# Kernel tuning notes

Hardware: AMD Instinct MI355X
Metric: run time of the kernel (lower is better)

The kernel has to match this reference:

```python
import jax, jax.numpy as jnp
import numpy as np

D_MODEL = 1024
NUM_HEADS = 16
D_K = D_MODEL // NUM_HEADS


def setup_inputs() -> dict:
    key = jax.random.key(0)
    ks = jax.random.split(key, 9)
    B, S = 2, 2048
    s_in = 1.0 / np.sqrt(D_MODEL)
    x = jax.random.normal(ks[0], (B, S, D_MODEL), dtype=jnp.float32)
    # Linear weights stored as (in_features, out_features): y = x @ W + b
    Wq = jax.random.uniform(ks[1], (D_MODEL, D_MODEL), jnp.float32, -s_in, s_in)
    bq = jax.random.uniform(ks[2], (D_MODEL,), jnp.float32, -s_in, s_in)
    Wk = jax.random.uniform(ks[3], (D_MODEL, D_K), jnp.float32, -s_in, s_in)
    bk = jax.random.uniform(ks[4], (D_K,), jnp.float32, -s_in, s_in)
    Wv = jax.random.uniform(ks[5], (D_MODEL, D_K), jnp.float32, -s_in, s_in)
    bv = jax.random.uniform(ks[6], (D_K,), jnp.float32, -s_in, s_in)
    Wo = jax.random.uniform(ks[7], (D_MODEL, D_MODEL), jnp.float32, -s_in, s_in)
    bo = jax.random.uniform(ks[8], (D_MODEL,), jnp.float32, -s_in, s_in)
    return {"x": x, "Wq": Wq, "bq": bq, "Wk": Wk, "bk": bk,
            "Wv": Wv, "bv": bv, "Wo": Wo, "bo": bo}


def reference(x, Wq, bq, Wk, bk, Wv, bv, Wo, bo):
    B, S, _ = x.shape
    H, Dk = NUM_HEADS, D_K
    # Projections
    Q = (x @ Wq + bq).reshape(B, S, H, Dk).transpose(0, 2, 1, 3)  # [B,H,S,Dk]
    K = x @ Wk + bk                                               # [B,S,Dk] single KV head
    V = x @ Wv + bv                                               # [B,S,Dk]
    # Scores: query heads broadcast against the single shared KV head
    scores = jnp.einsum('bhqd,bkd->bhqk', Q, K) / jnp.sqrt(jnp.float32(Dk))
    attn = jax.nn.softmax(scores, axis=-1)                        # [B,H,S,S]
    out = jnp.einsum('bhqk,bkd->bhqd', attn, V)                   # [B,H,S,Dk]
    out = out.transpose(0, 2, 1, 3).reshape(B, S, H * Dk)         # [B,S,d_model]
    return out @ Wo + bo
```

## Files before the change

### kernel.cpp

```cpp
#include <hip/hip_runtime.h>
#include <hip/hip_bf16.h>

typedef __attribute__((ext_vector_type(8))) short bf16x8;
typedef __attribute__((ext_vector_type(4))) float f32x4;
typedef __attribute__((ext_vector_type(16))) float f32x16;
typedef __attribute__((ext_vector_type(4))) unsigned short ushort4v;

#define QSCALE 0.1803368801111204f

__device__ __forceinline__ unsigned short f2bf(float f) {
  union { float f; unsigned int u; } x; x.f = f;
  unsigned int u = x.u;
  unsigned int r = (u + 0x7fffu + ((u >> 16) & 1u)) >> 16;
  return (unsigned short)r;
}

__device__ __forceinline__ void gll16(const unsigned short* g, unsigned short* l) {
  __builtin_amdgcn_global_load_lds(
      (const __attribute__((address_space(1))) unsigned int*)g,
      (__attribute__((address_space(3))) unsigned int*)l, 16, 0, 0);
}

__global__ __launch_bounds__(256) void prep_kernel(
    const float* __restrict__ x,
    const float* __restrict__ Wq, const float* __restrict__ Wk,
    const float* __restrict__ Wv, const float* __restrict__ Wo,
    unsigned short* __restrict__ xb,
    unsigned short* __restrict__ QKVt, unsigned short* __restrict__ Wot) {
  int z = blockIdx.z;
  if (z == 4) {
    size_t base = ((size_t)(blockIdx.y * 32 + blockIdx.x)) * 4096 + threadIdx.x * 16;
#pragma unroll
    for (int c = 0; c < 4; ++c) {
      float4 v = *(const float4*)(x + base + c * 4);
      ushort4v o = { f2bf(v.x), f2bf(v.y), f2bf(v.z), f2bf(v.w) };
      *(ushort4v*)(xb + base + c * 4) = o;
    }
    return;
  }
  __shared__ float t[32][33];
  const float* src;
  unsigned short* dst;
  int C, rowoff;
  if (z == 0)      { src = Wq; dst = QKVt; C = 1024; rowoff = 0; }
  else if (z == 1) { src = Wk; dst = QKVt; C = 64;   rowoff = 1024; }
  else if (z == 2) { src = Wv; dst = QKVt; C = 64;   rowoff = 1088; }
  else             { src = Wo; dst = Wot;  C = 1024; rowoff = 0; }
  int c0 = blockIdx.x * 32, r0 = blockIdx.y * 32;
  if (c0 >= C) return;
  int tx = threadIdx.x & 31, ty = threadIdx.x >> 5;
#pragma unroll
  for (int i = 0; i < 32; i += 8)
    t[ty + i][tx] = src[(size_t)(r0 + ty + i) * C + c0 + tx];
  __syncthreads();
#pragma unroll
  for (int i = 0; i < 32; i += 8)
    dst[(size_t)(rowoff + c0 + ty + i) * 1024 + r0 + tx] = f2bf(t[tx][ty + i]);
}

template <typename OutT, bool QKVMODE>
__global__ __launch_bounds__(256) void gemm_bf16_kernel(
    const unsigned short* __restrict__ A, const unsigned short* __restrict__ Bt,
    const float* __restrict__ b0, const float* __restrict__ b1,
    const float* __restrict__ b2, OutT* __restrict__ C,
    unsigned short* __restrict__ Vt, int M, int N, int K) {
  __shared__ __align__(16) unsigned short As[2][128 * 32];
  __shared__ __align__(16) unsigned short Bs[2][64 * 32];
  int tid = threadIdx.x;
  int wid = tid >> 6, lane = tid & 63;
  int l15 = lane & 15, quad = lane >> 4;
  int m0 = blockIdx.x * 128, n0 = blockIdx.y * 64;
  int mw = (wid >> 1) * 64, nw = (wid & 1) * 32;
  f32x4 acc[4][2];
#pragma unroll
  for (int i = 0; i < 4; i++)
#pragma unroll
    for (int j = 0; j < 2; j++)
#pragma unroll
      for (int e = 0; e < 4; ++e) acc[i][j][e] = 0.f;

  const unsigned short* Ag = A + (size_t)(m0 + (tid >> 2)) * K + (tid & 3) * 8;
  const unsigned short* Bg = Bt + (size_t)(n0 + (tid >> 2)) * K + (tid & 3) * 8;

  gll16(Ag, As[0] + tid * 8);
  gll16(Ag + (size_t)64 * K, As[0] + 2048 + tid * 8);
  gll16(Bg, Bs[0] + tid * 8);

  for (int k0 = 0; k0 < K; k0 += 32) {
    int cur = (k0 >> 5) & 1;
    if (k0 + 32 < K) {
      int nxt = cur ^ 1;
      gll16(Ag + k0 + 32, As[nxt] + tid * 8);
      gll16(Ag + (size_t)64 * K + k0 + 32, As[nxt] + 2048 + tid * 8);
      gll16(Bg + k0 + 32, Bs[nxt] + tid * 8);
      asm volatile("s_waitcnt vmcnt(3)" ::: "memory");
    } else {
      asm volatile("s_waitcnt vmcnt(0)" ::: "memory");
    }
    __builtin_amdgcn_s_barrier();
    __builtin_amdgcn_sched_barrier(0);
    const unsigned short* Asb = As[cur];
    const unsigned short* Bsb = Bs[cur];
    bf16x8 af[4], bfr[2];
#pragma unroll
    for (int t = 0; t < 4; ++t)
      af[t] = *(const bf16x8*)(Asb + (mw + t * 16 + l15) * 32 + quad * 8);
#pragma unroll
    for (int t = 0; t < 2; ++t)
      bfr[t] = *(const bf16x8*)(Bsb + (nw + t * 16 + l15) * 32 + quad * 8);
#pragma unroll
    for (int mt = 0; mt < 4; ++mt)
#pragma unroll
      for (int nt = 0; nt < 2; ++nt)
        acc[mt][nt] = __builtin_amdgcn_mfma_f32_16x16x32_bf16(
            af[mt], bfr[nt], acc[mt][nt], 0, 0, 0);
    asm volatile("s_waitcnt lgkmcnt(0)" ::: "memory");
    __builtin_amdgcn_sched_barrier(0);
    __builtin_amdgcn_s_barrier();
  }
#pragma unroll
  for (int mt = 0; mt < 4; ++mt)
#pragma unroll
    for (int nt = 0; nt < 2; ++nt) {
      int col = n0 + nw + nt * 16 + l15;
      float bias, cs;
      if constexpr (QKVMODE) {
        bias = (col < 1024) ? b0[col] : ((col < 1088) ? b1[col - 1024] : b2[col - 1088]);
        cs = (col < 1024) ? QSCALE : 1.0f;
      } else {
        bias = b0[col];
        cs = 1.0f;
      }
#pragma unroll
      for (int r = 0; r < 4; ++r) {
        int row = m0 + mw + mt * 16 + quad * 4 + r;
        float v = (acc[mt][nt][r] + bias) * cs;
        if constexpr (sizeof(OutT) == 2)
          C[(size_t)row * N + col] = f2bf(v);
        else
          C[(size_t)row * N + col] = v;
        if constexpr (QKVMODE) {
          if (col >= 1088)
            Vt[((size_t)(row >> 11) * 64 + (col - 1088)) * 2048 + (row & 2047)] =
                f2bf(v);
        }
      }
    }
}

__global__ __launch_bounds__(512, 4) void flash_attn_kernel(
    const unsigned short* __restrict__ QKV,
    const unsigned short* __restrict__ Vt,
    unsigned short* __restrict__ AO) {
  constexpr int S = 2048, LDQ = 1152;
  constexpr int PK = 72;
  __shared__ __align__(16) unsigned short smem[2][2][64 * PK];
  int tid = threadIdx.x;
  int wid = tid >> 6, lane = tid & 63;
  int l31 = lane & 31, half = lane >> 5;
  int p = wid & 3, ks = wid >> 2;
  int q0 = blockIdx.x * 128, h = blockIdx.y, b = blockIdx.z;

  const unsigned short* Qb =
      QKV + (size_t)(b * S + q0 + p * 32 + l31) * LDQ + h * 64 + half * 8;
  bf16x8 qf[4];
#pragma unroll
  for (int f = 0; f < 4; ++f) qf[f] = *(const bf16x8*)(Qb + f * 16);

  int u = tid & 255, sl = tid >> 8;
  int srow = u >> 2, sc = (u & 3) * 8;
  const unsigned short* Kgb = QKV + ((size_t)b * S) * LDQ + 1024;
  const unsigned short* Vgb = Vt + ((size_t)(b * 64 + srow)) * 2048;

  f32x16 oa0, oa1;
#pragma unroll
  for (int r = 0; r < 16; ++r) { oa0[r] = 0.f; oa1[r] = 0.f; }
  float rs = 0.f;

  int kb0 = sl * 1024;
  bf16x8 ka = *(const bf16x8*)(Kgb + (size_t)(kb0 + srow) * LDQ + sc);
  bf16x8 kc = *(const bf16x8*)(Kgb + (size_t)(kb0 + srow) * LDQ + sc + 32);
  bf16x8 va = *(const bf16x8*)(Vgb + kb0 + sc);
  bf16x8 vc = *(const bf16x8*)(Vgb + kb0 + sc + 32);

  unsigned short* Ksb = smem[ks][0];
  unsigned short* Vsb = smem[ks][1];

  for (int kt = 0; kt < 16; ++kt) {
    *(bf16x8*)(smem[sl][0] + srow * PK + sc) = ka;
    *(bf16x8*)(smem[sl][0] + srow * PK + sc + 32) = kc;
    *(bf16x8*)(smem[sl][1] + srow * PK + sc) = va;
    *(bf16x8*)(smem[sl][1] + srow * PK + sc + 32) = vc;
    __syncthreads();
    if (kt + 1 < 16) {
      int kbn = sl * 1024 + (kt + 1) * 64;
      ka = *(const bf16x8*)(Kgb + (size_t)(kbn + srow) * LDQ + sc);
      kc = *(const bf16x8*)(Kgb + (size_t)(kbn + srow) * LDQ + sc + 32);
      va = *(const bf16x8*)(Vgb + kbn + sc);
      vc = *(const bf16x8*)(Vgb + kbn + sc + 32);
    }

#pragma unroll
    for (int n2 = 0; n2 < 2; ++n2) {
      f32x16 sacc;
#pragma unroll
      for (int i = 0; i < 16; ++i) sacc[i] = 0.f;
#pragma unroll
      for (int s = 0; s < 4; ++s) {
        bf16x8 kf =
            *(const bf16x8*)(Ksb + (n2 * 32 + l31) * PK + s * 16 + half * 8);
        sacc = __builtin_amdgcn_mfma_f32_32x32x16_bf16(kf, qf[s], sacc, 0, 0, 0);
      }
#pragma unroll
      for (int t = 0; t < 2; ++t) {
        float pr[8];
#pragma unroll
        for (int j = 0; j < 8; ++j) {
          pr[j] = __builtin_amdgcn_exp2f(sacc[t * 8 + j]);
          rs += pr[j];
        }
        unsigned w0A, w1A, w0B, w1B;
        asm("v_cvt_pk_bf16_f32 %0, %1, %2" : "=v"(w0A) : "v"(pr[0]), "v"(pr[1]));
        asm("v_cvt_pk_bf16_f32 %0, %1, %2" : "=v"(w1A) : "v"(pr[2]), "v"(pr[3]));
        asm("v_cvt_pk_bf16_f32 %0, %1, %2" : "=v"(w0B) : "v"(pr[4]), "v"(pr[5]));
        asm("v_cvt_pk_bf16_f32 %0, %1, %2" : "=v"(w1B) : "v"(pr[6]), "v"(pr[7]));
        asm volatile("v_permlane32_swap_b32 %0, %1" : "+v"(w0A), "+v"(w0B));
        asm volatile("v_permlane32_swap_b32 %0, %1" : "+v"(w1A), "+v"(w1B));
        union { unsigned u[4]; bf16x8 v; } afu;
        afu.u[0] = w0A; afu.u[1] = w1A; afu.u[2] = w0B; afu.u[3] = w1B;
        int sg = n2 * 2 + t;
        bf16x8 vf0 = *(const bf16x8*)(Vsb + (l31) * PK + sg * 16 + half * 8);
        bf16x8 vf1 = *(const bf16x8*)(Vsb + (32 + l31) * PK + sg * 16 + half * 8);
        oa0 = __builtin_amdgcn_mfma_f32_32x32x16_bf16(afu.v, vf0, oa0, 0, 0, 0);
        oa1 = __builtin_amdgcn_mfma_f32_32x32x16_bf16(afu.v, vf1, oa1, 0, 0, 0);
      }
    }
    __syncthreads();
  }

  float rsf = rs + __shfl_xor(rs, 32, 64);

  float* Cb = (float*)smem;
  if (ks == 1) {
#pragma unroll
    for (int r = 0; r < 16; ++r) {
      int row = (r & 3) + 8 * (r >> 2) + 4 * half;
      Cb[(p * 32 + row) * 66 + l31] = oa0[r];
      Cb[(p * 32 + row) * 66 + 32 + l31] = oa1[r];
    }
    if (half == 0) Cb[(p * 32 + l31) * 66 + 64] = rsf;
  } else {
    if (half == 0) Cb[(p * 32 + l31) * 66 + 65] = rsf;
  }
  __syncthreads();
  if (ks == 0) {
    unsigned short* Ob = AO + (size_t)(b * S + q0 + p * 32) * 1024 + h * 64;
#pragma unroll
    for (int r = 0; r < 16; ++r) {
      int row = (r & 3) + 8 * (r >> 2) + 4 * half;
      float p0 = Cb[(p * 32 + row) * 66 + l31];
      float p1 = Cb[(p * 32 + row) * 66 + 32 + l31];
      float inv = 1.0f / (Cb[(p * 32 + row) * 66 + 64] + Cb[(p * 32 + row) * 66 + 65]);
      Ob[(size_t)row * 1024 + l31] = f2bf((oa0[r] + p0) * inv);
      Ob[(size_t)row * 1024 + 32 + l31] = f2bf((oa1[r] + p1) * inv);
    }
  }
}

extern "C" void kernel_launch(void* const* d_in, const int* in_sizes, int n_in,
                              void* d_out, int out_size, void* d_ws, size_t ws_size,
                              hipStream_t stream) {
  const float* x  = (const float*)d_in[0];
  const float* Wq = (const float*)d_in[1];
  const float* bq = (const float*)d_in[2];
  const float* Wk = (const float*)d_in[3];
  const float* bk = (const float*)d_in[4];
  const float* Wv = (const float*)d_in[5];
  const float* bv = (const float*)d_in[6];
  const float* Wo = (const float*)d_in[7];
  const float* bo = (const float*)d_in[8];
  float* out = (float*)d_out;

  constexpr int B = 2, S = 2048, D = 1024, Dk = 64, H = 16;
  constexpr int M = B * S;
  constexpr int NQKV = D + 2 * Dk;

  char* ws = (char*)d_ws;
  unsigned short* xb   = (unsigned short*)ws; ws += (size_t)M * D * 2;
  unsigned short* QKVt = (unsigned short*)ws; ws += (size_t)NQKV * D * 2;
  unsigned short* Wot  = (unsigned short*)ws; ws += (size_t)D * D * 2;
  unsigned short* QKV  = (unsigned short*)ws; ws += (size_t)M * NQKV * 2;
  unsigned short* Vtb  = (unsigned short*)ws; ws += (size_t)B * Dk * S * 2;
  unsigned short* AO   = (unsigned short*)ws; ws += (size_t)M * D * 2;

  prep_kernel<<<dim3(32, 32, 5), 256, 0, stream>>>(x, Wq, Wk, Wv, Wo, xb, QKVt, Wot);

  gemm_bf16_kernel<unsigned short, true><<<dim3(M / 128, NQKV / 64), 256, 0, stream>>>(
      xb, QKVt, bq, bk, bv, QKV, Vtb, M, NQKV, D);

  flash_attn_kernel<<<dim3(S / 128, H, B), 512, 0, stream>>>(QKV, Vtb, AO);

  gemm_bf16_kernel<float, false><<<dim3(M / 128, D / 64), 256, 0, stream>>>(
      AO, Wot, bo, nullptr, nullptr, out, nullptr, M, D, D);
}
```

Before: 173.3 us.

## Double-buffer K/V shared tiles with one barrier per tile and MFMA priority

Splits the K/V shared-memory staging into two ping-pong buffers. Global loads for tile t+2 are issued while tile t is computed, and the next buffer is written before a single barrier, replacing the two __syncthreads per tile. It also raises wave priority around the MFMA sections with s_setprio. This doubles LDS use per block (about 73 KB), which may limit how many blocks fit per CU, and it keeps more K/V registers live, adding register pressure.

```diff
diff --git a/kernel.cpp b/kernel.cpp
--- a/kernel.cpp
+++ b/kernel.cpp
@@ -154,7 +154,7 @@
     unsigned short* __restrict__ AO) {
   constexpr int S = 2048, LDQ = 1152;
   constexpr int PK = 72;
-  __shared__ __align__(16) unsigned short smem[2][2][64 * PK];
+  __shared__ __align__(16) unsigned short smem[2][2][2][64 * PK];
   int tid = threadIdx.x;
   int wid = tid >> 6, lane = tid & 63;
   int l31 = lane & 31, half = lane >> 5;
@@ -177,40 +177,45 @@
   for (int r = 0; r < 16; ++r) { oa0[r] = 0.f; oa1[r] = 0.f; }
   float rs = 0.f;
 
-  int kb0 = sl * 1024;
-  bf16x8 ka = *(const bf16x8*)(Kgb + (size_t)(kb0 + srow) * LDQ + sc);
-  bf16x8 kc = *(const bf16x8*)(Kgb + (size_t)(kb0 + srow) * LDQ + sc + 32);
-  bf16x8 va = *(const bf16x8*)(Vgb + kb0 + sc);
-  bf16x8 vc = *(const bf16x8*)(Vgb + kb0 + sc + 32);
-
-  unsigned short* Ksb = smem[ks][0];
-  unsigned short* Vsb = smem[ks][1];
-
-  for (int kt = 0; kt < 16; ++kt) {
-    *(bf16x8*)(smem[sl][0] + srow * PK + sc) = ka;
-    *(bf16x8*)(smem[sl][0] + srow * PK + sc + 32) = kc;
-    *(bf16x8*)(smem[sl][1] + srow * PK + sc) = va;
-    *(bf16x8*)(smem[sl][1] + srow * PK + sc + 32) = vc;
-    __syncthreads();
-    if (kt + 1 < 16) {
-      int kbn = sl * 1024 + (kt + 1) * 64;
-      ka = *(const bf16x8*)(Kgb + (size_t)(kbn + srow) * LDQ + sc);
-      kc = *(const bf16x8*)(Kgb + (size_t)(kbn + srow) * LDQ + sc + 32);
-      va = *(const bf16x8*)(Vgb + kbn + sc);
-      vc = *(const bf16x8*)(Vgb + kbn + sc + 32);
-    }
-
+#define LOADT(RA, RC, VA, VC, kt)                                          \
+  do {                                                                     \
+    int kb_ = sl * 1024 + (kt) * 64;                                       \
+    RA = *(const bf16x8*)(Kgb + (size_t)(kb_ + srow) * LDQ + sc);          \
+    RC = *(const bf16x8*)(Kgb + (size_t)(kb_ + srow) * LDQ + sc + 32);     \
+    VA = *(const bf16x8*)(Vgb + kb_ + sc);                                 \
+    VC = *(const bf16x8*)(Vgb + kb_ + sc + 32);                            \
+  } while (0)
+
+#define WRITET(bi, RA, RC, VA, VC)                                         \
+  do {                                                                     \
+    *(bf16x8*)(smem[bi][sl][0] + srow * PK + sc) = RA;                     \
+    *(bf16x8*)(smem[bi][sl][0] + srow * PK + sc + 32) = RC;                \
+    *(bf16x8*)(smem[bi][sl][1] + srow * PK + sc) = VA;                     \
+    *(bf16x8*)(smem[bi][sl][1] + srow * PK + sc + 32) = VC;                \
+  } while (0)
+
+#define BAR()                                                              \
+  do {                                                                     \
+    asm volatile("s_waitcnt lgkmcnt(0)" ::: "memory");                     \
+    __builtin_amdgcn_sched_barrier(0);                                     \
+    __builtin_amdgcn_s_barrier();                                          \
+    __builtin_amdgcn_sched_barrier(0);                                     \
+  } while (0)
+
+  auto compute = [&](const unsigned short* Ksb, const unsigned short* Vsb) {
 #pragma unroll
     for (int n2 = 0; n2 < 2; ++n2) {
       f32x16 sacc;
 #pragma unroll
       for (int i = 0; i < 16; ++i) sacc[i] = 0.f;
+      __builtin_amdgcn_s_setprio(1);
 #pragma unroll
       for (int s = 0; s < 4; ++s) {
         bf16x8 kf =
             *(const bf16x8*)(Ksb + (n2 * 32 + l31) * PK + s * 16 + half * 8);
         sacc = __builtin_amdgcn_mfma_f32_32x32x16_bf16(kf, qf[s], sacc, 0, 0, 0);
       }
+      __builtin_amdgcn_s_setprio(0);
 #pragma unroll
       for (int t = 0; t < 2; ++t) {
         float pr[8];
@@ -231,12 +236,36 @@
         int sg = n2 * 2 + t;
         bf16x8 vf0 = *(const bf16x8*)(Vsb + (l31) * PK + sg * 16 + half * 8);
         bf16x8 vf1 = *(const bf16x8*)(Vsb + (32 + l31) * PK + sg * 16 + half * 8);
+        __builtin_amdgcn_s_setprio(1);
         oa0 = __builtin_amdgcn_mfma_f32_32x32x16_bf16(afu.v, vf0, oa0, 0, 0, 0);
         oa1 = __builtin_amdgcn_mfma_f32_32x32x16_bf16(afu.v, vf1, oa1, 0, 0, 0);
+        __builtin_amdgcn_s_setprio(0);
       }
     }
-    __syncthreads();
-  }
+  };
+
+  bf16x8 ka0, kc0, va0, vc0, ka1, kc1, va1, vc1;
+
+  LOADT(ka0, kc0, va0, vc0, 0);
+  WRITET(0, ka0, kc0, va0, vc0);
+  LOADT(ka1, kc1, va1, vc1, 1);
+  BAR();
+
+#pragma unroll 1
+  for (int kp = 0; kp < 8; ++kp) {
+    int t0 = kp * 2;
+    if (t0 + 2 < 16) LOADT(ka0, kc0, va0, vc0, t0 + 2);
+    compute(smem[0][ks][0], smem[0][ks][1]);
+    WRITET(1, ka1, kc1, va1, vc1);
+    BAR();
+    if (t0 + 3 < 16) LOADT(ka1, kc1, va1, vc1, t0 + 3);
+    compute(smem[1][ks][0], smem[1][ks][1]);
+    if (t0 + 2 < 16) WRITET(0, ka0, kc0, va0, vc0);
+    BAR();
+  }
+#undef LOADT
+#undef WRITET
+#undef BAR
 
   float rsf = rs + __shfl_xor(rs, 32, 64);
 
```

Result: slower. 243.7 us (+40.6%).
